# Kernel optimization log

Measured on AMD Instinct MI355X. Metric: run time of the kernel, lower is better.

The kernel has to match this reference:

```python
import jax, jax.numpy as jnp
import numpy as np

L, D, N_E = 32768, 64, 16384
BETA = 0.25
EMBED_INIT_SCALE = 1.0


def setup_inputs() -> dict:
    key = jax.random.key(0)
    k1, k2 = jax.random.split(key)
    z = jax.random.normal(k1, (L, D), dtype=jnp.float32)
    # nn.Embedding initialized uniform(-embed_init_scale/n_e, embed_init_scale/n_e)
    embedding = jax.random.uniform(
        k2, (N_E, D), dtype=jnp.float32,
        minval=-EMBED_INIT_SCALE / N_E, maxval=EMBED_INIT_SCALE / N_E)
    return {"z": z, "embedding": embedding}


def reference(z, embedding):
    # Euclidean distance: d[l, n] = ||z_l||^2 + ||e_n||^2 - 2 <z_l, e_n>   -> (L, N)
    d = (jnp.sum(z * z, axis=1, keepdims=True)
         + jnp.sum(embedding * embedding, axis=1)
         - 2.0 * jnp.einsum('ld,nd->ln', z, embedding))
    # get_index with gumbel disabled: indices = argmax(-d) == argmin(d)
    indices = jnp.argmin(d, axis=1)                      # (L,) int
    # codebook lookup (one-hot matmul == gather)
    z_q = jnp.take(embedding, indices, axis=0)           # (L, D)
    # VQ loss: beta * ||z - sg[e]||^2 + ||sg[z] - e||^2
    sg = jax.lax.stop_gradient
    loss = (BETA * jnp.mean((sg(z_q) - z) ** 2)
            + jnp.mean((z_q - sg(z)) ** 2))
    # straight-through estimator
    z_q_st = z + sg(z_q - z)
    return z_q_st, loss, indices
```

## Files before the change

kernel.cpp:

```cpp
#include <hip/hip_runtime.h>
#include <cstdint>
#include <cstddef>

#define L_TOK 32768
#define D_DIM 64
#define NE    16384
#define GCHUNKS 8
#define NPB   (NE / GCHUNKS)
#define BN    128
#define NCH   (NPB / BN)
#define WROWS 32
#define BROWS 256
#define RBLOCKS  (L_TOK / 32)

#define ASCALE  -4194304.0f
#define ESCALE   2097152.0f
#define KBIAS_F  32768.0f
#define QDELTA   160u

typedef unsigned short ushort_t;
typedef __attribute__((ext_vector_type(8))) short bf16x8;
typedef __attribute__((ext_vector_type(4))) float f32x4;

#define WS_EHI   0u
#define WS_ESQ32 (2u<<20)
#define WS_ESQS  ((2u<<20) + (64u<<10))
#define WS_ESQ64 ((2u<<20) + (128u<<10))
#define WS_CAND  ((2u<<20) + (256u<<10))
#define WS_PART  ((6u<<20) + (256u<<10))

__device__ __forceinline__ ushort_t bf16_rne(float v) {
  unsigned u = __float_as_uint(v);
  return (ushort_t)((u + 0x7fffu + ((u >> 16) & 1u)) >> 16);
}

__device__ __forceinline__ unsigned umed3(unsigned a, unsigned b, unsigned c) {
  unsigned d;
  asm("v_med3_u32 %0, %1, %2, %3" : "=v"(d) : "v"(a), "v"(b), "v"(c));
  return d;
}

__device__ __forceinline__ void load_lds16(const ushort_t* g, ushort_t* l) {
  __builtin_amdgcn_global_load_lds(
      (const __attribute__((address_space(1))) void*)g,
      (__attribute__((address_space(3))) void*)l, 16, 0, 0);
}

__device__ __forceinline__ float np_sum64(float a) {
  int j = threadIdx.x & 7;
  float r = __shfl(a, j);
  #pragma unroll
  for (int m = 1; m < 8; ++m) r += __shfl(a, j + 8 * m);
  float s0 = __shfl(r, 0), s1 = __shfl(r, 1), s2 = __shfl(r, 2), s3 = __shfl(r, 3);
  float s4 = __shfl(r, 4), s5 = __shfl(r, 5), s6 = __shfl(r, 6), s7 = __shfl(r, 7);
  return ((s0 + s1) + (s2 + s3)) + ((s4 + s5) + (s6 + s7));
}

__device__ __forceinline__ int perm_off(int n, int k) {
  int tile = n >> 4, c = n & 15, s = k >> 5, q = (k >> 3) & 3, j = k & 7;
  return tile * 1024 + s * 512 + (q * 16 + c) * 8 + j;
}

__global__ __launch_bounds__(256) void vq_prep_e(const float* __restrict__ e,
                                                 ushort_t* __restrict__ ehi,
                                                 float* __restrict__ esq32,
                                                 float* __restrict__ esqs,
                                                 double* __restrict__ esq64) {
  int wave = threadIdx.x >> 6, lane = threadIdx.x & 63;
  int row = blockIdx.x * 4 + wave;
  float v = e[(size_t)row * D_DIM + lane];
  ehi[perm_off(row, lane)] = bf16_rne(v);
  float esq = np_sum64(v * v);
  double p = (double)v * (double)v;
  #pragma unroll
  for (int o = 32; o; o >>= 1) p += __shfl_xor(p, o);
  if (lane == 0) {
    esq32[row] = esq;
    esqs[row]  = esq * ESCALE + KBIAS_F;
    esq64[row] = p;
  }
}

__global__ __launch_bounds__(512, 8) void vq_argmin(const float* __restrict__ z,
                                                    const ushort_t* __restrict__ ehi,
                                                    const float* __restrict__ esqs,
                                                    unsigned* __restrict__ candk) {
  __shared__ __align__(16) unsigned char smem[40960];
  ushort_t* s_buf = (ushort_t*)smem;
  float*    s_esq = (float*)(smem + 32768);

  const int tid = threadIdx.x;
  const int wave = tid >> 6, lane = tid & 63;
  const int q = lane >> 4, c = lane & 15;
  const int row0 = blockIdx.y * BROWS + wave * WROWS;
  const int nbase = blockIdx.x * NPB;

  bf16x8 zA[2][2];
  #pragma unroll
  for (int g = 0; g < 2; ++g) {
    const float* zr = z + (size_t)(row0 + g * 16 + c) * D_DIM;
    float4 a0 = *(const float4*)(zr + q * 8);
    float4 a1 = *(const float4*)(zr + q * 8 + 4);
    float4 a2 = *(const float4*)(zr + 32 + q * 8);
    float4 a3 = *(const float4*)(zr + 32 + q * 8 + 4);
    zA[g][0][0] = (short)bf16_rne(a0.x * ASCALE); zA[g][0][1] = (short)bf16_rne(a0.y * ASCALE);
    zA[g][0][2] = (short)bf16_rne(a0.z * ASCALE); zA[g][0][3] = (short)bf16_rne(a0.w * ASCALE);
    zA[g][0][4] = (short)bf16_rne(a1.x * ASCALE); zA[g][0][5] = (short)bf16_rne(a1.y * ASCALE);
    zA[g][0][6] = (short)bf16_rne(a1.z * ASCALE); zA[g][0][7] = (short)bf16_rne(a1.w * ASCALE);
    zA[g][1][0] = (short)bf16_rne(a2.x * ASCALE); zA[g][1][1] = (short)bf16_rne(a2.y * ASCALE);
    zA[g][1][2] = (short)bf16_rne(a2.z * ASCALE); zA[g][1][3] = (short)bf16_rne(a2.w * ASCALE);
    zA[g][1][4] = (short)bf16_rne(a3.x * ASCALE); zA[g][1][5] = (short)bf16_rne(a3.y * ASCALE);
    zA[g][1][6] = (short)bf16_rne(a3.z * ASCALE); zA[g][1][7] = (short)bf16_rne(a3.w * ASCALE);
  }

  ((float4*)s_esq)[tid] = ((const float4*)(esqs + nbase))[tid];

  unsigned K0[2][4], K1[2][4];
  #pragma unroll
  for (int g = 0; g < 2; ++g)
    #pragma unroll
    for (int r = 0; r < 4; ++r) { K0[g][r] = 0xFFFFFFFFu; K1[g][r] = 0xFFFFFFFFu; }

  {
    const ushort_t* g = ehi + (size_t)nbase * 64 + wave * 1024 + lane * 8;
    ushort_t* l = s_buf + wave * 1024 + lane * 8;
    load_lds16(g, l);
    load_lds16(g + 512, l + 512);
  }

  for (int cb = 0; cb < NCH; ++cb) {
    __syncthreads();
    if (cb + 1 < NCH) {
      int nnext = nbase + (cb + 1) * BN;
      const ushort_t* g = ehi + (size_t)nnext * 64 + wave * 1024 + lane * 8;
      ushort_t* l = s_buf + ((cb + 1) & 1) * 8192 + wave * 1024 + lane * 8;
      load_lds16(g, l);
      load_lds16(g + 512, l + 512);
    }
    const ushort_t* buf = s_buf + (cb & 1) * 8192;
    const float*    esqc = s_esq + cb * BN;

    #pragma unroll
    for (int t = 0; t < BN / 16; ++t) {
      const bf16x8 bh0 = *(const bf16x8*)(buf + t * 1024 + lane * 8);
      const bf16x8 bh1 = *(const bf16x8*)(buf + t * 1024 + 512 + lane * 8);
      float esqv = esqc[t * 16 + c];
      f32x4 cvec = {esqv, esqv, esqv, esqv};
      unsigned tcv = (((unsigned)(cb * 8 + t)) << 4) | (unsigned)c;
      f32x4 acc0 = __builtin_amdgcn_mfma_f32_16x16x32_bf16(zA[0][0], bh0, cvec, 0, 0, 0);
      acc0 = __builtin_amdgcn_mfma_f32_16x16x32_bf16(zA[0][1], bh1, acc0, 0, 0, 0);
      f32x4 acc1 = __builtin_amdgcn_mfma_f32_16x16x32_bf16(zA[1][0], bh0, cvec, 0, 0, 0);
      acc1 = __builtin_amdgcn_mfma_f32_16x16x32_bf16(zA[1][1], bh1, acc1, 0, 0, 0);
      #pragma unroll
      for (int r = 0; r < 4; ++r) {
        unsigned pk = (((unsigned)acc0[r]) << 12) | tcv;
        K1[0][r] = umed3(pk, K0[0][r], K1[0][r]);
        K0[0][r] = min(pk, K0[0][r]);
      }
      #pragma unroll
      for (int r = 0; r < 4; ++r) {
        unsigned pk = (((unsigned)acc1[r]) << 12) | tcv;
        K1[1][r] = umed3(pk, K0[1][r], K1[1][r]);
        K0[1][r] = min(pk, K0[1][r]);
      }
    }
  }

  __syncthreads();
  unsigned* s_k = (unsigned*)smem;
  #pragma unroll
  for (int g = 0; g < 2; ++g)
    #pragma unroll
    for (int r = 0; r < 4; ++r) {
      int rowidx = wave * WROWS + g * 16 + q * 4 + r;
      int base = rowidx * 36 + c * 2;
      s_k[base + 0] = K0[g][r]; s_k[base + 1] = K1[g][r];
    }
  __syncthreads();
  if (tid < BROWS) {
    unsigned M0 = 0xFFFFFFFFu, M1 = 0xFFFFFFFFu, M2 = 0xFFFFFFFFu, M3 = 0xFFFFFFFFu;
    const uint4* sv = (const uint4*)(s_k + tid * 36);
    #pragma unroll
    for (int v4 = 0; v4 < 8; ++v4) {
      uint4 kk = sv[v4];
      unsigned vals[4] = {kk.x, kk.y, kk.z, kk.w};
      #pragma unroll
      for (int u = 0; u < 4; ++u) {
        unsigned v = vals[u];
        M3 = umed3(v, M2, M3);
        M2 = umed3(v, M1, M2);
        M1 = umed3(v, M0, M1);
        M0 = min(v, M0);
      }
    }
    int grow = blockIdx.y * BROWS + tid;
    unsigned* cp = candk + ((size_t)blockIdx.x * L_TOK + grow) * 4;
    cp[0] = M0; cp[1] = M1; cp[2] = M2; cp[3] = M3;
  }
}

__global__ __launch_bounds__(512, 6) void vq_refine(const float* __restrict__ z,
                                                    const float* __restrict__ e,
                                                    const float* __restrict__ esq32,
                                                    const double* __restrict__ esq64,
                                                    const unsigned* __restrict__ candk,
                                                    float* __restrict__ out,
                                                    double* __restrict__ partials) {
  const int tid = threadIdx.x;
  const int wave = tid >> 6, lane = tid & 63;
  const int g = lane >> 1, s = lane & 1;
  __shared__ double sp[8];
  double wl = 0.0;
  for (int it = 0; it < 4; ++it) {
    int row = blockIdx.x * 32 + wave * 4 + it;
    float zf = z[(size_t)row * D_DIM + lane];
    float zsqv = np_sum64(zf * zf);
    double zp64 = (double)zf * (double)zf;
    #pragma unroll
    for (int o = 32; o; o >>= 1) zp64 += __shfl_xor(zp64, o);
    unsigned k = candk[((size_t)(g >> 2) * L_TOK + row) * 4 + (g & 3)];
    unsigned qi = k >> 12;
    unsigned n  = ((unsigned)(g >> 2) * (unsigned)NPB) + (k & 4095u);
    unsigned gkey = (qi << 14) | n;
    unsigned m = gkey;
    #pragma unroll
    for (int o = 1; o < 64; o <<= 1) m = min(m, (unsigned)__shfl_xor((int)m, o));
    unsigned minqi = m >> 14;
    bool part = qi <= minqi + QDELTA;
    unsigned long long key = ~0ull;
    double dotw = 0.0;
    if (part) {
      const float4* ep = (const float4*)(e + (size_t)n * D_DIM + s * 32);
      const float4* zp = (const float4*)(z + (size_t)row * D_DIM + s * 32);
      double da = 0.0, db = 0.0, dc = 0.0, dd = 0.0;
      #pragma unroll
      for (int h = 0; h < 2; ++h) {
        float4 e0 = ep[h * 4 + 0], e1 = ep[h * 4 + 1];
        float4 e2 = ep[h * 4 + 2], e3 = ep[h * 4 + 3];
        float4 z0 = zp[h * 4 + 0], z1 = zp[h * 4 + 1];
        float4 z2 = zp[h * 4 + 2], z3 = zp[h * 4 + 3];
        da = fma((double)e0.x, (double)z0.x, da); da = fma((double)e0.y, (double)z0.y, da);
        da = fma((double)e0.z, (double)z0.z, da); da = fma((double)e0.w, (double)z0.w, da);
        db = fma((double)e1.x, (double)z1.x, db); db = fma((double)e1.y, (double)z1.y, db);
        db = fma((double)e1.z, (double)z1.z, db); db = fma((double)e1.w, (double)z1.w, db);
        dc = fma((double)e2.x, (double)z2.x, dc); dc = fma((double)e2.y, (double)z2.y, dc);
        dc = fma((double)e2.z, (double)z2.z, dc); dc = fma((double)e2.w, (double)z2.w, dc);
        dd = fma((double)e3.x, (double)z3.x, dd); dd = fma((double)e3.y, (double)z3.y, dd);
        dd = fma((double)e3.z, (double)z3.z, dd); dd = fma((double)e3.w, (double)z3.w, dd);
      }
      double dot = (da + db) + (dc + dd);
      dot += __shfl_xor(dot, 1);
      float t2 = (float)(2.0 * dot);
      float T1 = zsqv + esq32[n];
      float d  = T1 - t2;
      key  = ((unsigned long long)__float_as_uint(d) << 14) | n;
      dotw = dot;
    }
    #pragma unroll
    for (int o = 2; o <= 32; o <<= 1) {
      unsigned long long ok = __shfl_xor(key, o);
      double od = __shfl_xor(dotw, o);
      bool take = ok < key;
      key  = take ? ok : key;
      dotw = take ? od : dotw;
    }
    int win = (int)(key & 16383u);
    float be = e[(size_t)win * D_DIM + lane];
    out[(size_t)row * D_DIM + lane] = zf + (be - zf);
    if (lane == 0) {
      out[(size_t)L_TOK * D_DIM + 1 + row] = (float)win;
      wl += zp64 + esq64[win] - 2.0 * dotw;
    }
  }
  if (lane == 0) sp[wave] = wl;
  __syncthreads();
  if (tid == 0) {
    double t = 0.0;
    #pragma unroll
    for (int w = 0; w < 8; ++w) t += sp[w];
    partials[blockIdx.x] = t;
  }
}

__global__ __launch_bounds__(512) void vq_loss(const double* __restrict__ partials,
                                               float* __restrict__ out) {
  int tid = threadIdx.x;
  double v = partials[tid] + partials[tid + 512];
  #pragma unroll
  for (int o = 32; o; o >>= 1) v += __shfl_xor(v, o);
  __shared__ double sp[8];
  if ((tid & 63) == 0) sp[tid >> 6] = v;
  __syncthreads();
  if (tid == 0) {
    double tot = 0.0;
    #pragma unroll
    for (int w = 0; w < 8; ++w) tot += sp[w];
    out[(size_t)L_TOK * D_DIM] = (float)(1.25 * tot / (double)((size_t)L_TOK * D_DIM));
  }
}

extern "C" void kernel_launch(void* const* d_in, const int* in_sizes, int n_in,
                              void* d_out, int out_size, void* d_ws, size_t ws_size,
                              hipStream_t stream) {
  const float* z = (const float*)d_in[0];
  const float* e = (const float*)d_in[1];
  float* out = (float*)d_out;
  char* ws = (char*)d_ws;

  ushort_t* ehi   = (ushort_t*)(ws + WS_EHI);
  float*    esq32 = (float*)(ws + WS_ESQ32);
  float*    esqs  = (float*)(ws + WS_ESQS);
  double*   esq64 = (double*)(ws + WS_ESQ64);
  unsigned* candk = (unsigned*)(ws + WS_CAND);
  double*   parts = (double*)(ws + WS_PART);

  vq_prep_e<<<NE / 4, 256, 0, stream>>>(e, ehi, esq32, esqs, esq64);
  vq_argmin<<<dim3(GCHUNKS, L_TOK / BROWS), 512, 0, stream>>>(z, ehi, esqs, candk);
  vq_refine<<<RBLOCKS, 512, 0, stream>>>(z, e, esq32, esq64, candk, out, parts);
  vq_loss<<<1, 512, 0, stream>>>(parts, out);
}
```

Measured before the change: 205.1 us.

## Precompute z norms in prep, transpose candidate layout, compute loss directly

The prep kernel now also computes fp32 squared norms of z, so the refine kernel no longer does per-row shuffle reductions, including an fp64 one. The candidate buffer is transposed to row-major (row, chunk, slot), so each row's 32 candidates are contiguous and load coalesced in refine. The loss is now accumulated as the squared difference between the selected codeword and z in double, which removes the esq64 table and the shuffling of the dot product alongside the key. The cost is an extra pass over z in prep and a changed rounding path for the loss.

```diff
diff --git a/kernel.cpp b/kernel.cpp
--- a/kernel.cpp
+++ b/kernel.cpp
@@ -12,6 +12,8 @@
 #define WROWS 32
 #define BROWS 256
 #define RBLOCKS  (L_TOK / 32)
+#define EBLK  (NE / 4)
+#define ZBLK  (L_TOK / 4)
 
 #define ASCALE  -4194304.0f
 #define ESCALE   2097152.0f
@@ -25,7 +27,7 @@
 #define WS_EHI   0u
 #define WS_ESQ32 (2u<<20)
 #define WS_ESQS  ((2u<<20) + (64u<<10))
-#define WS_ESQ64 ((2u<<20) + (128u<<10))
+#define WS_ZSQ32 ((2u<<20) + (128u<<10))
 #define WS_CAND  ((2u<<20) + (256u<<10))
 #define WS_PART  ((6u<<20) + (256u<<10))
 
@@ -61,23 +63,27 @@
   return tile * 1024 + s * 512 + (q * 16 + c) * 8 + j;
 }
 
-__global__ __launch_bounds__(256) void vq_prep_e(const float* __restrict__ e,
-                                                 ushort_t* __restrict__ ehi,
-                                                 float* __restrict__ esq32,
-                                                 float* __restrict__ esqs,
-                                                 double* __restrict__ esq64) {
+__global__ __launch_bounds__(256) void vq_prep(const float* __restrict__ e,
+                                               const float* __restrict__ z,
+                                               ushort_t* __restrict__ ehi,
+                                               float* __restrict__ esq32,
+                                               float* __restrict__ esqs,
+                                               float* __restrict__ zsq32) {
   int wave = threadIdx.x >> 6, lane = threadIdx.x & 63;
-  int row = blockIdx.x * 4 + wave;
-  float v = e[(size_t)row * D_DIM + lane];
-  ehi[perm_off(row, lane)] = bf16_rne(v);
-  float esq = np_sum64(v * v);
-  double p = (double)v * (double)v;
-  #pragma unroll
-  for (int o = 32; o; o >>= 1) p += __shfl_xor(p, o);
-  if (lane == 0) {
-    esq32[row] = esq;
-    esqs[row]  = esq * ESCALE + KBIAS_F;
-    esq64[row] = p;
+  if (blockIdx.x < EBLK) {
+    int row = blockIdx.x * 4 + wave;
+    float v = e[(size_t)row * D_DIM + lane];
+    ehi[perm_off(row, lane)] = bf16_rne(v);
+    float esq = np_sum64(v * v);
+    if (lane == 0) {
+      esq32[row] = esq;
+      esqs[row]  = esq * ESCALE + KBIAS_F;
+    }
+  } else {
+    int row = (blockIdx.x - EBLK) * 4 + wave;
+    float v = z[(size_t)row * D_DIM + lane];
+    float s = np_sum64(v * v);
+    if (lane == 0) zsq32[row] = s;
   }
 }
 
@@ -194,7 +200,7 @@
       }
     }
     int grow = blockIdx.y * BROWS + tid;
-    unsigned* cp = candk + ((size_t)blockIdx.x * L_TOK + grow) * 4;
+    unsigned* cp = candk + ((size_t)grow * GCHUNKS + blockIdx.x) * 4;
     cp[0] = M0; cp[1] = M1; cp[2] = M2; cp[3] = M3;
   }
 }
@@ -202,7 +208,7 @@
 __global__ __launch_bounds__(512, 6) void vq_refine(const float* __restrict__ z,
                                                     const float* __restrict__ e,
                                                     const float* __restrict__ esq32,
-                                                    const double* __restrict__ esq64,
+                                                    const float* __restrict__ zsq32,
                                                     const unsigned* __restrict__ candk,
                                                     float* __restrict__ out,
                                                     double* __restrict__ partials) {
@@ -214,13 +220,10 @@
   for (int it = 0; it < 4; ++it) {
     int row = blockIdx.x * 32 + wave * 4 + it;
     float zf = z[(size_t)row * D_DIM + lane];
-    float zsqv = np_sum64(zf * zf);
-    double zp64 = (double)zf * (double)zf;
-    #pragma unroll
-    for (int o = 32; o; o >>= 1) zp64 += __shfl_xor(zp64, o);
-    unsigned k = candk[((size_t)(g >> 2) * L_TOK + row) * 4 + (g & 3)];
+    float zsqv = zsq32[row];
+    unsigned k = candk[(size_t)row * 32 + g];
     unsigned qi = k >> 12;
-    unsigned n  = ((unsigned)(g >> 2) * (unsigned)NPB) + (k & 4095u);
+    unsigned n  = ((unsigned)(g >> 2)) * (unsigned)NPB + (k & 4095u);
     unsigned gkey = (qi << 14) | n;
     unsigned m = gkey;
     #pragma unroll
@@ -228,7 +231,6 @@
     unsigned minqi = m >> 14;
     bool part = qi <= minqi + QDELTA;
     unsigned long long key = ~0ull;
-    double dotw = 0.0;
     if (part) {
       const float4* ep = (const float4*)(e + (size_t)n * D_DIM + s * 32);
       const float4* zp = (const float4*)(z + (size_t)row * D_DIM + s * 32);
@@ -254,24 +256,21 @@
       float T1 = zsqv + esq32[n];
       float d  = T1 - t2;
       key  = ((unsigned long long)__float_as_uint(d) << 14) | n;
-      dotw = dot;
     }
     #pragma unroll
     for (int o = 2; o <= 32; o <<= 1) {
       unsigned long long ok = __shfl_xor(key, o);
-      double od = __shfl_xor(dotw, o);
-      bool take = ok < key;
-      key  = take ? ok : key;
-      dotw = take ? od : dotw;
+      key = ok < key ? ok : key;
     }
     int win = (int)(key & 16383u);
     float be = e[(size_t)win * D_DIM + lane];
     out[(size_t)row * D_DIM + lane] = zf + (be - zf);
-    if (lane == 0) {
-      out[(size_t)L_TOK * D_DIM + 1 + row] = (float)win;
-      wl += zp64 + esq64[win] - 2.0 * dotw;
-    }
-  }
+    if (lane == 0) out[(size_t)L_TOK * D_DIM + 1 + row] = (float)win;
+    double dd2 = (double)be - (double)zf;
+    wl += dd2 * dd2;
+  }
+  #pragma unroll
+  for (int o = 32; o; o >>= 1) wl += __shfl_xor(wl, o);
   if (lane == 0) sp[wave] = wl;
   __syncthreads();
   if (tid == 0) {
@@ -310,12 +309,12 @@
   ushort_t* ehi   = (ushort_t*)(ws + WS_EHI);
   float*    esq32 = (float*)(ws + WS_ESQ32);
   float*    esqs  = (float*)(ws + WS_ESQS);
-  double*   esq64 = (double*)(ws + WS_ESQ64);
+  float*    zsq32 = (float*)(ws + WS_ZSQ32);
   unsigned* candk = (unsigned*)(ws + WS_CAND);
   double*   parts = (double*)(ws + WS_PART);
 
-  vq_prep_e<<<NE / 4, 256, 0, stream>>>(e, ehi, esq32, esqs, esq64);
+  vq_prep<<<EBLK + ZBLK, 256, 0, stream>>>(e, z, ehi, esq32, esqs, zsq32);
   vq_argmin<<<dim3(GCHUNKS, L_TOK / BROWS), 512, 0, stream>>>(z, ehi, esqs, candk);
-  vq_refine<<<RBLOCKS, 512, 0, stream>>>(z, e, esq32, esq64, candk, out, parts);
+  vq_refine<<<RBLOCKS, 512, 0, stream>>>(z, e, esq32, zsq32, candk, out, parts);
   vq_loss<<<1, 512, 0, stream>>>(parts, out);
 }
```

Result: no change. 203.6 us (-0.7%).
